# Performance work log

Hardware: AMD Instinct MI355X
Metric: run time of the kernel (lower is better)

The kernel has to match this reference:

```python
import jax, jax.numpy as jnp
import numpy as np

N_NODES = 50000
N_EDGES = 1_600_000
Q_MULT = 8          # charges_irreps = 8x0e
NODE_MULT = 64      # node_feat_irreps = 64x0e + 64x1o
RBF = 8             # edge_feats_irreps num_irreps
HID = 64            # FullyConnectedNet hidden width
W_NUMEL = 2 * Q_MULT  # edge_tp weight_numel: two uvu paths (0e->0e, 0e x 1o->1o), u=8


def setup_inputs() -> dict:
    key = jax.random.key(0)
    k = jax.random.split(key, 14)
    f = lambda kk, sh: jax.random.normal(kk, sh, dtype=jnp.float32)
    return {
        "node_feats": f(k[0], (N_NODES, NODE_MULT * 4)),          # 64 scalars + 64 vectors(3)
        "charges_0": f(k[1], (N_NODES, Q_MULT)),                  # unused in forward
        "charges_induced": f(k[2], (N_NODES, Q_MULT)),
        "edge_feats": f(k[3], (N_EDGES, RBF)),
        "edge_attrs": f(k[4], (N_EDGES, 4)),                      # Y0 (1) + Y1 (3)
        "field_feats": f(k[5], (N_NODES, RBF)),                   # unused in forward
        "mlp_w1": f(k[6], (RBF, HID)),
        "mlp_w2": f(k[7], (HID, HID)),
        "mlp_w3": f(k[8], (HID, HID)),
        "mlp_w4": f(k[9], (HID, W_NUMEL)),
        "W0": f(k[10], (Q_MULT, NODE_MULT)),                      # node_tp path 0e x 0e -> 0e
        "W1": f(k[11], (Q_MULT, NODE_MULT)),                      # node_tp path 1o x 1o -> 0e
        "edge_index": jax.random.randint(k[12], (2, N_EDGES), 0, N_NODES, dtype=jnp.int32),
        "batch": jnp.zeros((N_NODES,), dtype=jnp.int32),
    }


def reference(node_feats, charges_0, charges_induced, edge_feats, edge_attrs,
              field_feats, mlp_w1, mlp_w2, mlp_w3, mlp_w4, W0, W1,
              edge_index, batch):
    sender, receiver = edge_index[0], edge_index[1]
    num_nodes = node_feats.shape[0]

    # e3nn FullyConnectedNet: variance-normalized linear layers + silu
    h = edge_feats
    for w in (mlp_w1, mlp_w2, mlp_w3):
        h = jax.nn.silu(h @ (w / np.sqrt(np.float32(w.shape[0]))))
    tp_w = h @ (mlp_w4 / np.sqrt(np.float32(mlp_w4.shape[0])))   # [E, 16]
    w0, w1 = tp_w[:, :Q_MULT], tp_w[:, Q_MULT:]                   # per-edge path weights

    # edge_tp (uvu, external weights): gather sender charges, weighted CG product
    q_s = charges_induced[sender]                                  # [E, 8]
    mid0 = (w0 * q_s) * edge_attrs[:, :1]                          # [E, 8]    0e
    mid1 = (w1 * q_s)[:, :, None] * edge_attrs[:, None, 1:4]       # [E, 8, 3] 1o

    # scatter-sum messages to receiver nodes
    sum0 = jax.ops.segment_sum(mid0, receiver, num_segments=num_nodes)
    sum1 = jax.ops.segment_sum(mid1.reshape(-1, Q_MULT * 3), receiver,
                               num_segments=num_nodes).reshape(-1, Q_MULT, 3)

    # node_tp: FullyConnectedTensorProduct(8x0e+8x1o, 64x0e+64x1o -> 1x0e)
    node0 = node_feats[:, :NODE_MULT]                              # [N, 64]
    node1 = node_feats[:, NODE_MULT:].reshape(-1, NODE_MULT, 3)    # [N, 64, 3]
    c = 1.0 / np.sqrt(np.float32(Q_MULT * NODE_MULT * 2))          # path normalization
    e0 = jnp.einsum('nu,nv,uv->n', sum0, node0, W0)
    e1 = jnp.einsum('nuk,nvk,uv->n', sum1, node1, W1) / np.sqrt(np.float32(3.0))  # w3j(1,1,0)
    return c * (e0 + e1)                                           # [N] per-node energy
```

## Files before the change

kernel.cpp:

```cpp
#include <hip/hip_runtime.h>
#include <hip/hip_bf16.h>

typedef short short8 __attribute__((ext_vector_type(8)));
typedef float f32x4 __attribute__((ext_vector_type(4)));

static __device__ __forceinline__ float bf2f(unsigned int b) { return __uint_as_float(b << 16); }
static __device__ __forceinline__ short fb2s(float x) {
    unsigned u = __float_as_uint(x);
    return (short)((u + 0x7FFFu + ((u >> 16) & 1u)) >> 16);
}
static __device__ __forceinline__ unsigned int pack2(float lo, float hi) {
    unsigned int r;
    asm("v_cvt_pk_bf16_f32 %0, %1, %2" : "=v"(r) : "v"(lo), "v"(hi));
    return r;
}
static __device__ __forceinline__ float hsilu(float y) {
    return y * __builtin_amdgcn_rcpf(1.0f + __builtin_amdgcn_exp2f(-y));
}
static __device__ __forceinline__ float load1(const void* p, long off, int isbf) {
    return isbf ? bf2f(((const unsigned short*)p)[off]) : ((const float*)p)[off];
}
static __device__ __forceinline__ void load4(const void* p, long off, int isbf, float* o) {
    if (isbf) {
        uint2 v = *(const uint2*)((const unsigned short*)p + off);
        o[0]=bf2f(v.x&0xffffu); o[1]=bf2f(v.x>>16);
        o[2]=bf2f(v.y&0xffffu); o[3]=bf2f(v.y>>16);
    } else {
        float4 v = *(const float4*)((const float*)p + off);
        o[0]=v.x; o[1]=v.y; o[2]=v.z; o[3]=v.w;
    }
}
static __device__ __forceinline__ int detect_bf16(const void* nf) {
    const unsigned int* w = (const unsigned int*)nf;
    int lane = threadIdx.x & 63;
    unsigned int e = (w[lane] >> 7) & 0xFFu;
    unsigned long long m = __ballot(e >= 118u && e <= 132u);
    return __popcll(m) >= 32 ? 1 : 0;
}

#define NB 32
__global__ __launch_bounds__(256) void k_node(
    const void* __restrict__ nf, const void* __restrict__ W0, const void* __restrict__ W1,
    const void* __restrict__ w1, const void* __restrict__ w2,
    const void* __restrict__ w3, const void* __restrict__ w4,
    short* __restrict__ Bws, float* __restrict__ NA, float* __restrict__ acc, int n_nodes) {
    __shared__ float Nd0[NB * 68];
    __shared__ float Nd1[3 * NB * 68];
    __shared__ float W0L[8 * 68];
    __shared__ float W1L[8 * 68];
    const int tid = threadIdx.x;
    const int isbf = detect_bf16(nf);
    const long n0 = (long)blockIdx.x * NB;

    if (blockIdx.x < 44) {
        int idx = blockIdx.x * 256 + tid;
        int j = idx & 7, lane = (idx >> 3) & 63, tile = idx >> 9;
        int n16 = lane & 15, kq = lane >> 4;
        float v;
        if (tile < 4) {
            int k = kq * 8 + j, n = tile * 16 + n16;
            v = (k < 8) ? load1(w1, k * 64 + n, isbf) * (0.35355339059327373f * 1.4426950408889634f) : 0.0f;
        } else if (tile < 12) {
            int t = (tile - 4) >> 1, kt = (tile - 4) & 1;
            int k = kt * 32 + kq * 8 + j, n = t * 16 + n16;
            v = load1(w2, k * 64 + n, isbf) * 0.125f;
        } else if (tile < 20) {
            int t = (tile - 12) >> 1, kt = (tile - 12) & 1;
            int k = kt * 32 + kq * 8 + j, n = t * 16 + n16;
            v = load1(w3, k * 64 + n, isbf) * 0.125f;
        } else {
            int kt = tile - 20;
            int k = kt * 32 + kq * 8 + j, n = n16;
            v = load1(w4, k * 16 + n, isbf) * (0.125f * 0.6931471805599453f);
        }
        Bws[idx] = fb2s(v);
    }
    if (tid < NB) {
        long n = n0 + tid;
        if (n < n_nodes) acc[n] = 0.0f;
    }
    if (n0 >= n_nodes) return;

    for (int i = tid; i < 512; i += 256) {
        W0L[(i >> 6) * 68 + (i & 63)] = load1(W0, i, isbf);
        W1L[(i >> 6) * 68 + (i & 63)] = load1(W1, i, isbf);
    }
    if (isbf) {
        for (int i = tid; i < NB * 32; i += 256) {
            int node = i >> 5, c8 = (i & 31) * 8;
            long ng = n0 + node; if (ng > n_nodes - 1) ng = n_nodes - 1;
            uint4 v = *(const uint4*)((const unsigned short*)nf + ng * 256 + c8);
            float f[8];
            f[0]=bf2f(v.x&0xffffu); f[1]=bf2f(v.x>>16);
            f[2]=bf2f(v.y&0xffffu); f[3]=bf2f(v.y>>16);
            f[4]=bf2f(v.z&0xffffu); f[5]=bf2f(v.z>>16);
            f[6]=bf2f(v.w&0xffffu); f[7]=bf2f(v.w>>16);
            #pragma unroll
            for (int t = 0; t < 8; t++) {
                int col = c8 + t;
                if (col < 64) Nd0[node * 68 + col] = f[t];
                else {
                    int cc = col - 64, vv = cc / 3, kk = cc - vv * 3;
                    Nd1[(kk * NB + node) * 68 + vv] = f[t];
                }
            }
        }
    } else {
        for (int i = tid; i < NB * 64; i += 256) {
            int node = i >> 6, c4 = (i & 63) * 4;
            long ng = n0 + node; if (ng > n_nodes - 1) ng = n_nodes - 1;
            float4 v = *(const float4*)((const float*)nf + ng * 256 + c4);
            float f[4] = {v.x, v.y, v.z, v.w};
            #pragma unroll
            for (int t = 0; t < 4; t++) {
                int col = c4 + t;
                if (col < 64) Nd0[node * 68 + col] = f[t];
                else {
                    int cc = col - 64, vv = cc / 3, kk = cc - vv * 3;
                    Nd1[(kk * NB + node) * 68 + vv] = f[t];
                }
            }
        }
    }
    __syncthreads();

    const int wv = tid >> 6, lane = tid & 63;
    const int u = lane & 7, ln = lane >> 3;
    float sum[4] = {0.0f, 0.0f, 0.0f, 0.0f};

    if (wv == 0) {
        const float* w = &W0L[u * 68];
        for (int v0 = 0; v0 < 64; v0 += 4) {
            float4 w4 = *(const float4*)(w + v0);
            #pragma unroll
            for (int j = 0; j < 4; j++) {
                float4 nd = *(const float4*)&Nd0[(ln + 8 * j) * 68 + v0];
                sum[j] += w4.x * nd.x + w4.y * nd.y + w4.z * nd.z + w4.w * nd.w;
            }
        }
        #pragma unroll
        for (int j = 0; j < 4; j++) {
            long node = n0 + ln + 8 * j;
            if (node < n_nodes) NA[node * 32 + u] = sum[j] * 0.03125f;
        }
    } else {
        const int kk = wv - 1;
        const float* w = &W1L[u * 68];
        const float* nd1 = &Nd1[kk * NB * 68];
        for (int v0 = 0; v0 < 64; v0 += 4) {
            float4 w4 = *(const float4*)(w + v0);
            #pragma unroll
            for (int j = 0; j < 4; j++) {
                float4 nd = *(const float4*)&nd1[(ln + 8 * j) * 68 + v0];
                sum[j] += w4.x * nd.x + w4.y * nd.y + w4.z * nd.z + w4.w * nd.w;
            }
        }
        #pragma unroll
        for (int j = 0; j < 4; j++) {
            long node = n0 + ln + 8 * j;
            if (node < n_nodes) NA[node * 32 + 8 + u * 3 + kk] = sum[j] * 0.018042195912175804f;
        }
    }
}

__global__ __launch_bounds__(256, 5) void k_edges_mfma(
    const void* __restrict__ ef, const void* __restrict__ ea, const void* __restrict__ qc,
    const int* __restrict__ eidx, const void* __restrict__ nf,
    const short* __restrict__ Bws, const float* __restrict__ NA,
    float* __restrict__ acc, int n_edges) {
    __shared__ __align__(16) short W[11264];
    __shared__ __align__(16) short Hs[4 * 1152];
    const int tid = threadIdx.x, lane = tid & 63, wv = tid >> 6;
    const int n16 = lane & 15, kq = lane >> 4;
    const int isbf = detect_bf16(nf);

    {
        const uint4* src = (const uint4*)Bws;
        uint4* dst = (uint4*)W;
        for (int i = tid; i < 1408; i += 256) dst[i] = src[i];
    }
    __syncthreads();

    short* Hw = Hs + wv * 1152;
    const int rbit = (n16 >> 3) & 1;
    const int wrow = n16 * 72 + ((kq & 1) << 2);
    const int kql = (kq & 1) << 2;
    const f32x4 zero = {0.0f, 0.0f, 0.0f, 0.0f};

    for (int half = 0; half < 2; half++) {
        #pragma unroll
        for (int nt = 0; nt < 2; nt++) {
            const long E0 = (long)blockIdx.x * 256 + half * 128 + wv * 32 + nt * 16;
            const long e = E0 + n16;
            long ec = e; if (ec > n_edges - 1) ec = n_edges - 1;

            const int s_nd = eidx[ec];
            const int r_nd = eidx[(long)n_edges + ec];
            float eav[4];
            load4(ea, ec * 4, isbf, eav);

            short8 a1 = {0,0,0,0,0,0,0,0};
            if (kq == 0) {
                if (isbf) {
                    a1 = *(const short8*)((const unsigned short*)ef + ec * 8);
                } else {
                    const float* pe = (const float*)ef + ec * 8;
                    float4 v0 = *(const float4*)pe, v1 = *(const float4*)(pe + 4);
                    a1[0]=fb2s(v0.x); a1[1]=fb2s(v0.y); a1[2]=fb2s(v0.z); a1[3]=fb2s(v0.w);
                    a1[4]=fb2s(v1.x); a1[5]=fb2s(v1.y); a1[6]=fb2s(v1.z); a1[7]=fb2s(v1.w);
                }
            }

            {
                f32x4 c1[4];
                #pragma unroll
                for (int t = 0; t < 4; t++) {
                    short8 b = *(const short8*)(W + t * 512 + lane * 8);
                    c1[t] = __builtin_amdgcn_mfma_f32_16x16x32_bf16(b, a1, zero, 0, 0, 0);
                }
                #pragma unroll
                for (int t = 0; t < 4; t++) {
                    uint2 pkd;
                    pkd.x = pack2(hsilu(c1[t][0]), hsilu(c1[t][1]));
                    pkd.y = pack2(hsilu(c1[t][2]), hsilu(c1[t][3]));
                    *(uint2*)(Hw + wrow + (((t * 2 + (kq >> 1)) ^ rbit) << 3)) = pkd;
                }
            }

            float q4[4];
            load4(qc, (long)s_nd * 8 + kql, isbf, q4);
            float na[12];
            const float* nr = NA + (long)r_nd * 32;
            if (kq < 2) {
                *(float4*)na = *(const float4*)(nr + (kq << 2));
            } else {
                *(float4*)(na + 0) = *(const float4*)(nr + 8 + (kq - 2) * 12);
                *(float4*)(na + 4) = *(const float4*)(nr + 12 + (kq - 2) * 12);
                *(float4*)(na + 8) = *(const float4*)(nr + 16 + (kq - 2) * 12);
            }

            #pragma unroll
            for (int L = 0; L < 2; L++) {
                const int base = (L == 0) ? 4 : 12;
                short8 aH[2];
                #pragma unroll
                for (int kt = 0; kt < 2; kt++)
                    aH[kt] = *(const short8*)(Hw + n16 * 72 + (((kt * 4 + kq) ^ rbit) << 3));
                f32x4 c2[4];
                #pragma unroll
                for (int t = 0; t < 4; t++) c2[t] = zero;
                #pragma unroll
                for (int kt = 0; kt < 2; kt++)
                    #pragma unroll
                    for (int t = 0; t < 4; t++) {
                        short8 b = *(const short8*)(W + (base + t * 2 + kt) * 512 + lane * 8);
                        c2[t] = __builtin_amdgcn_mfma_f32_16x16x32_bf16(b, aH[kt], c2[t], 0, 0, 0);
                    }
                #pragma unroll
                for (int t = 0; t < 4; t++) {
                    uint2 pkd;
                    pkd.x = pack2(hsilu(c2[t][0]), hsilu(c2[t][1]));
                    pkd.y = pack2(hsilu(c2[t][2]), hsilu(c2[t][3]));
                    *(uint2*)(Hw + wrow + (((t * 2 + (kq >> 1)) ^ rbit) << 3)) = pkd;
                }
            }

            f32x4 c4 = zero;
            {
                short8 aH[2];
                #pragma unroll
                for (int kt = 0; kt < 2; kt++)
                    aH[kt] = *(const short8*)(Hw + n16 * 72 + (((kt * 4 + kq) ^ rbit) << 3));
                #pragma unroll
                for (int kt = 0; kt < 2; kt++) {
                    short8 b = *(const short8*)(W + (20 + kt) * 512 + lane * 8);
                    c4 = __builtin_amdgcn_mfma_f32_16x16x32_bf16(b, aH[kt], c4, 0, 0, 0);
                }
            }

            {
                float p = 0.0f;
                if (kq < 2) {
                    #pragma unroll
                    for (int r = 0; r < 4; r++) p += c4[r] * q4[r] * na[r];
                    p *= eav[0];
                } else {
                    #pragma unroll
                    for (int r = 0; r < 4; r++) {
                        float d = eav[1] * na[r * 3] + eav[2] * na[r * 3 + 1] + eav[3] * na[r * 3 + 2];
                        p += c4[r] * q4[r] * d;
                    }
                }
                p += __shfl_xor(p, 16);
                p += __shfl_xor(p, 32);
                if (kq == 0 && e < n_edges) atomicAdd(&acc[r_nd], p);
            }
        }
    }
}

__global__ void k_out(const float* __restrict__ acc, void* __restrict__ out,
                      const void* __restrict__ nf, int n) {
    const int isbf = detect_bf16(nf);
    int i = blockIdx.x * 256 + threadIdx.x;
    if (i >= n) return;
    if (isbf) ((__hip_bfloat16*)out)[i] = __float2bfloat16(acc[i]);
    else      ((float*)out)[i] = acc[i];
}

extern "C" void kernel_launch(void* const* d_in, const int* in_sizes, int n_in,
                              void* d_out, int out_size, void* d_ws, size_t ws_size,
                              hipStream_t stream) {
    const void* node_feats      = d_in[0];
    const void* charges_induced = d_in[2];
    const void* edge_feats      = d_in[3];
    const void* edge_attrs      = d_in[4];
    const void* mlp_w1          = d_in[6];
    const void* mlp_w2          = d_in[7];
    const void* mlp_w3          = d_in[8];
    const void* mlp_w4          = d_in[9];
    const void* W0              = d_in[10];
    const void* W1              = d_in[11];
    const int*  edge_index      = (const int*)d_in[12];

    const int n_nodes = in_sizes[0] / 256;
    const int n_edges = in_sizes[3] / 8;

    short* Bws = (short*)d_ws;
    float* NA  = (float*)((char*)d_ws + 22528);
    float* acc = NA + (size_t)n_nodes * 32;

    int nblk = (n_nodes + NB - 1) / NB;
    if (nblk < 44) nblk = 44;
    k_node<<<nblk, 256, 0, stream>>>(node_feats, W0, W1,
        mlp_w1, mlp_w2, mlp_w3, mlp_w4, Bws, NA, acc, n_nodes);
    k_edges_mfma<<<(n_edges + 255) / 256, 256, 0, stream>>>(
        edge_feats, edge_attrs, charges_induced, edge_index, node_feats, Bws, NA, acc, n_edges);
    k_out<<<(n_nodes + 255) / 256, 256, 0, stream>>>(acc, d_out, node_feats, n_nodes);
}
```

Before: 320.4 us.

## Process two 16-edge MFMA tiles jointly per wave to reuse weight fragments

Restructures the per-wave edge loop so both 16-edge tiles are handled together. Each weight fragment loaded from LDS now feeds two MFMAs, and the two independent MFMA chains can interleave to hide latency. The per-wave hidden-state scratch buffer is doubled and launch bounds are lowered from 5 to 4 blocks per SM to make room for the extra registers and LDS. The cost is lower occupancy, which may expose more of the gather and atomic latency.

```diff
diff --git a/kernel.cpp b/kernel.cpp
--- a/kernel.cpp
+++ b/kernel.cpp
@@ -163,13 +163,13 @@
     }
 }
 
-__global__ __launch_bounds__(256, 5) void k_edges_mfma(
+__global__ __launch_bounds__(256, 4) void k_edges_mfma(
     const void* __restrict__ ef, const void* __restrict__ ea, const void* __restrict__ qc,
     const int* __restrict__ eidx, const void* __restrict__ nf,
     const short* __restrict__ Bws, const float* __restrict__ NA,
     float* __restrict__ acc, int n_edges) {
     __shared__ __align__(16) short W[11264];
-    __shared__ __align__(16) short Hs[4 * 1152];
+    __shared__ __align__(16) short Hs[4 * 2304];
     const int tid = threadIdx.x, lane = tid & 63, wv = tid >> 6;
     const int n16 = lane & 15, kq = lane >> 4;
     const int isbf = detect_bf16(nf);
@@ -181,120 +181,146 @@
     }
     __syncthreads();
 
-    short* Hw = Hs + wv * 1152;
+    short* Hw = Hs + wv * 2304;
     const int rbit = (n16 >> 3) & 1;
     const int wrow = n16 * 72 + ((kq & 1) << 2);
     const int kql = (kq & 1) << 2;
     const f32x4 zero = {0.0f, 0.0f, 0.0f, 0.0f};
 
     for (int half = 0; half < 2; half++) {
-        #pragma unroll
-        for (int nt = 0; nt < 2; nt++) {
-            const long E0 = (long)blockIdx.x * 256 + half * 128 + wv * 32 + nt * 16;
-            const long e = E0 + n16;
-            long ec = e; if (ec > n_edges - 1) ec = n_edges - 1;
-
-            const int s_nd = eidx[ec];
-            const int r_nd = eidx[(long)n_edges + ec];
-            float eav[4];
-            load4(ea, ec * 4, isbf, eav);
-
-            short8 a1 = {0,0,0,0,0,0,0,0};
+        const long E0 = (long)blockIdx.x * 256 + half * 128 + wv * 32;
+
+        long e_[2]; long ec_[2]; int s_[2], r_[2]; float eav_[2][4];
+        #pragma unroll
+        for (int mt = 0; mt < 2; mt++) {
+            e_[mt] = E0 + mt * 16 + n16;
+            long ec = e_[mt]; if (ec > n_edges - 1) ec = n_edges - 1;
+            ec_[mt] = ec;
+            s_[mt] = eidx[ec];
+            r_[mt] = eidx[(long)n_edges + ec];
+            load4(ea, ec * 4, isbf, eav_[mt]);
+        }
+
+        short8 a1[2];
+        #pragma unroll
+        for (int mt = 0; mt < 2; mt++) {
+            short8 a = {0,0,0,0,0,0,0,0};
             if (kq == 0) {
                 if (isbf) {
-                    a1 = *(const short8*)((const unsigned short*)ef + ec * 8);
+                    a = *(const short8*)((const unsigned short*)ef + ec_[mt] * 8);
                 } else {
-                    const float* pe = (const float*)ef + ec * 8;
+                    const float* pe = (const float*)ef + ec_[mt] * 8;
                     float4 v0 = *(const float4*)pe, v1 = *(const float4*)(pe + 4);
-                    a1[0]=fb2s(v0.x); a1[1]=fb2s(v0.y); a1[2]=fb2s(v0.z); a1[3]=fb2s(v0.w);
-                    a1[4]=fb2s(v1.x); a1[5]=fb2s(v1.y); a1[6]=fb2s(v1.z); a1[7]=fb2s(v1.w);
-                }
-            }
-
-            {
-                f32x4 c1[4];
-                #pragma unroll
-                for (int t = 0; t < 4; t++) {
-                    short8 b = *(const short8*)(W + t * 512 + lane * 8);
-                    c1[t] = __builtin_amdgcn_mfma_f32_16x16x32_bf16(b, a1, zero, 0, 0, 0);
-                }
+                    a[0]=fb2s(v0.x); a[1]=fb2s(v0.y); a[2]=fb2s(v0.z); a[3]=fb2s(v0.w);
+                    a[4]=fb2s(v1.x); a[5]=fb2s(v1.y); a[6]=fb2s(v1.z); a[7]=fb2s(v1.w);
+                }
+            }
+            a1[mt] = a;
+        }
+
+        {
+            f32x4 c1[2][4];
+            #pragma unroll
+            for (int t = 0; t < 4; t++) {
+                short8 b = *(const short8*)(W + t * 512 + lane * 8);
+                #pragma unroll
+                for (int mt = 0; mt < 2; mt++)
+                    c1[mt][t] = __builtin_amdgcn_mfma_f32_16x16x32_bf16(b, a1[mt], zero, 0, 0, 0);
+            }
+            #pragma unroll
+            for (int mt = 0; mt < 2; mt++)
                 #pragma unroll
                 for (int t = 0; t < 4; t++) {
                     uint2 pkd;
-                    pkd.x = pack2(hsilu(c1[t][0]), hsilu(c1[t][1]));
-                    pkd.y = pack2(hsilu(c1[t][2]), hsilu(c1[t][3]));
-                    *(uint2*)(Hw + wrow + (((t * 2 + (kq >> 1)) ^ rbit) << 3)) = pkd;
-                }
-            }
-
-            float q4[4];
-            load4(qc, (long)s_nd * 8 + kql, isbf, q4);
-            float na[12];
-            const float* nr = NA + (long)r_nd * 32;
+                    pkd.x = pack2(hsilu(c1[mt][t][0]), hsilu(c1[mt][t][1]));
+                    pkd.y = pack2(hsilu(c1[mt][t][2]), hsilu(c1[mt][t][3]));
+                    *(uint2*)(Hw + mt * 1152 + wrow + (((t * 2 + (kq >> 1)) ^ rbit) << 3)) = pkd;
+                }
+        }
+
+        float q4_[2][4], na_[2][12];
+        #pragma unroll
+        for (int mt = 0; mt < 2; mt++) {
+            load4(qc, (long)s_[mt] * 8 + kql, isbf, q4_[mt]);
+            const float* nr = NA + (long)r_[mt] * 32;
             if (kq < 2) {
-                *(float4*)na = *(const float4*)(nr + (kq << 2));
+                *(float4*)na_[mt] = *(const float4*)(nr + (kq << 2));
             } else {
-                *(float4*)(na + 0) = *(const float4*)(nr + 8 + (kq - 2) * 12);
-                *(float4*)(na + 4) = *(const float4*)(nr + 12 + (kq - 2) * 12);
-                *(float4*)(na + 8) = *(const float4*)(nr + 16 + (kq - 2) * 12);
-            }
-
-            #pragma unroll
-            for (int L = 0; L < 2; L++) {
-                const int base = (L == 0) ? 4 : 12;
-                short8 aH[2];
+                *(float4*)(na_[mt] + 0) = *(const float4*)(nr + 8 + (kq - 2) * 12);
+                *(float4*)(na_[mt] + 4) = *(const float4*)(nr + 12 + (kq - 2) * 12);
+                *(float4*)(na_[mt] + 8) = *(const float4*)(nr + 16 + (kq - 2) * 12);
+            }
+        }
+
+        #pragma unroll
+        for (int L = 0; L < 2; L++) {
+            const int base = (L == 0) ? 4 : 12;
+            short8 aH[2][2];
+            #pragma unroll
+            for (int mt = 0; mt < 2; mt++)
                 #pragma unroll
                 for (int kt = 0; kt < 2; kt++)
-                    aH[kt] = *(const short8*)(Hw + n16 * 72 + (((kt * 4 + kq) ^ rbit) << 3));
-                f32x4 c2[4];
-                #pragma unroll
-                for (int t = 0; t < 4; t++) c2[t] = zero;
-                #pragma unroll
-                for (int kt = 0; kt < 2; kt++)
+                    aH[mt][kt] = *(const short8*)(Hw + mt * 1152 + n16 * 72 + (((kt * 4 + kq) ^ rbit) << 3));
+            f32x4 c2[2][4];
+            #pragma unroll
+            for (int mt = 0; mt < 2; mt++)
+                #pragma unroll
+                for (int t = 0; t < 4; t++) c2[mt][t] = zero;
+            #pragma unroll
+            for (int kt = 0; kt < 2; kt++)
+                #pragma unroll
+                for (int t = 0; t < 4; t++) {
+                    short8 b = *(const short8*)(W + (base + t * 2 + kt) * 512 + lane * 8);
                     #pragma unroll
-                    for (int t = 0; t < 4; t++) {
-                        short8 b = *(const short8*)(W + (base + t * 2 + kt) * 512 + lane * 8);
-                        c2[t] = __builtin_amdgcn_mfma_f32_16x16x32_bf16(b, aH[kt], c2[t], 0, 0, 0);
-                    }
+                    for (int mt = 0; mt < 2; mt++)
+                        c2[mt][t] = __builtin_amdgcn_mfma_f32_16x16x32_bf16(b, aH[mt][kt], c2[mt][t], 0, 0, 0);
+                }
+            #pragma unroll
+            for (int mt = 0; mt < 2; mt++)
                 #pragma unroll
                 for (int t = 0; t < 4; t++) {
                     uint2 pkd;
-                    pkd.x = pack2(hsilu(c2[t][0]), hsilu(c2[t][1]));
-                    pkd.y = pack2(hsilu(c2[t][2]), hsilu(c2[t][3]));
-                    *(uint2*)(Hw + wrow + (((t * 2 + (kq >> 1)) ^ rbit) << 3)) = pkd;
-                }
-            }
-
-            f32x4 c4 = zero;
-            {
-                short8 aH[2];
+                    pkd.x = pack2(hsilu(c2[mt][t][0]), hsilu(c2[mt][t][1]));
+                    pkd.y = pack2(hsilu(c2[mt][t][2]), hsilu(c2[mt][t][3]));
+                    *(uint2*)(Hw + mt * 1152 + wrow + (((t * 2 + (kq >> 1)) ^ rbit) << 3)) = pkd;
+                }
+        }
+
+        f32x4 c4[2] = {zero, zero};
+        {
+            short8 aH[2][2];
+            #pragma unroll
+            for (int mt = 0; mt < 2; mt++)
                 #pragma unroll
                 for (int kt = 0; kt < 2; kt++)
-                    aH[kt] = *(const short8*)(Hw + n16 * 72 + (((kt * 4 + kq) ^ rbit) << 3));
-                #pragma unroll
-                for (int kt = 0; kt < 2; kt++) {
-                    short8 b = *(const short8*)(W + (20 + kt) * 512 + lane * 8);
-                    c4 = __builtin_amdgcn_mfma_f32_16x16x32_bf16(b, aH[kt], c4, 0, 0, 0);
-                }
-            }
-
-            {
-                float p = 0.0f;
-                if (kq < 2) {
-                    #pragma unroll
-                    for (int r = 0; r < 4; r++) p += c4[r] * q4[r] * na[r];
-                    p *= eav[0];
-                } else {
-                    #pragma unroll
-                    for (int r = 0; r < 4; r++) {
-                        float d = eav[1] * na[r * 3] + eav[2] * na[r * 3 + 1] + eav[3] * na[r * 3 + 2];
-                        p += c4[r] * q4[r] * d;
-                    }
-                }
-                p += __shfl_xor(p, 16);
-                p += __shfl_xor(p, 32);
-                if (kq == 0 && e < n_edges) atomicAdd(&acc[r_nd], p);
-            }
+                    aH[mt][kt] = *(const short8*)(Hw + mt * 1152 + n16 * 72 + (((kt * 4 + kq) ^ rbit) << 3));
+            #pragma unroll
+            for (int kt = 0; kt < 2; kt++) {
+                short8 b = *(const short8*)(W + (20 + kt) * 512 + lane * 8);
+                #pragma unroll
+                for (int mt = 0; mt < 2; mt++)
+                    c4[mt] = __builtin_amdgcn_mfma_f32_16x16x32_bf16(b, aH[mt][kt], c4[mt], 0, 0, 0);
+            }
+        }
+
+        #pragma unroll
+        for (int mt = 0; mt < 2; mt++) {
+            float p = 0.0f;
+            if (kq < 2) {
+                #pragma unroll
+                for (int r = 0; r < 4; r++) p += c4[mt][r] * q4_[mt][r] * na_[mt][r];
+                p *= eav_[mt][0];
+            } else {
+                #pragma unroll
+                for (int r = 0; r < 4; r++) {
+                    float d = eav_[mt][1] * na_[mt][r * 3] + eav_[mt][2] * na_[mt][r * 3 + 1]
+                            + eav_[mt][3] * na_[mt][r * 3 + 2];
+                    p += c4[mt][r] * q4_[mt][r] * d;
+                }
+            }
+            p += __shfl_xor(p, 16);
+            p += __shfl_xor(p, 32);
+            if (kq == 0 && e_[mt] < n_edges) atomicAdd(&acc[r_[mt]], p);
         }
     }
 }
```

Result: slower. 378.8 us (+18.2%).
